# Optimization experiments

Hardware: AMD Instinct MI355X
Metric: run time of the kernel (lower is better)

Reference implementation:

```python
import jax, jax.numpy as jnp
import numpy as np

ALPHA_LINK = 2.0   # init arg alpha_link
TOP_K = 4096       # init arg top_k
BATCH = 65536
NUM_CLASSES = 4096


def setup_inputs() -> dict:
    key = jax.random.key(0)
    k1, k2, k3 = jax.random.split(key, 3)
    y_pred = jax.random.normal(k1, (BATCH, NUM_CLASSES), dtype=jnp.float32)
    y_true = jax.random.randint(k2, (BATCH,), 0, NUM_CLASSES, dtype=jnp.int32)
    # dense boolean link table: link_table[gt, pred] == True iff pred in link[gt]
    link_table = jax.random.randint(k3, (NUM_CLASSES, NUM_CLASSES), 0, 2, dtype=jnp.int32).astype(bool)
    return {"y_pred": y_pred, "y_true": y_true, "link_table": link_table}


def reference(y_pred, y_true, link_table):
    # vectorized replacement of the per-sample dict-lookup loop
    pred = jnp.argmax(y_pred, axis=1)                     # [B]
    linked = link_table[y_true, pred]                     # [B] bool
    # factor = alpha_link iff pred != gt and pred in link[gt]; else 1
    factor = jnp.where((pred != y_true) & linked, ALPHA_LINK, 1.0)
    # cross_entropy(reduction='none'), weight=None
    logp = jax.nn.log_softmax(y_pred, axis=1)             # [B, C]
    ce = -jnp.take_along_axis(logp, y_true[:, None], axis=1)[:, 0]  # [B]
    worst_k, _ = jax.lax.top_k(factor * ce, TOP_K)        # [TOP_K]
    return jnp.mean(worst_k)
```

## Files before the change

### kernel.cpp

```cpp
#include <hip/hip_runtime.h>

#define NCLS   4096
#define BATCHN 65536
#define TOPK   4096
#define ALPHA  2.0f

typedef float vfloat4 __attribute__((ext_vector_type(4)));

__global__ __launch_bounds__(256) void detect_and_zero_kernel(
    const unsigned int* __restrict__ lt, int* __restrict__ flag,
    unsigned int* __restrict__ ghist) {
    const int tid = threadIdx.x;
    #pragma unroll
    for (int i = 0; i < 16; ++i) ghist[i * 256 + tid] = 0u;
    if (tid < 64) {
        unsigned int bad = 0;
        for (int i = tid; i < 1024; i += 64) bad |= (lt[i] > 1u) ? 1u : 0u;
        unsigned long long mask = __ballot(bad != 0);
        if (tid == 0) flag[0] = (mask == 0ULL) ? 1 : 0;
    }
}

__device__ inline void amax_comb(float& m, int& mi, float om, int omi) {
    if (om > m || (om == m && omi < mi)) { m = om; mi = omi; }
}

__global__ __launch_bounds__(256) void row_loss_kernel(
    const float* __restrict__ yp, const int* __restrict__ yt,
    const unsigned char* __restrict__ lt, const int* __restrict__ flag,
    float* __restrict__ losses) {
    const int b   = blockIdx.x;
    const int tid = threadIdx.x;
    const vfloat4* row = reinterpret_cast<const vfloat4*>(yp + (size_t)b * NCLS);

    vfloat4 v0 = __builtin_nontemporal_load(&row[0 * 256 + tid]);
    vfloat4 v1 = __builtin_nontemporal_load(&row[1 * 256 + tid]);
    vfloat4 v2 = __builtin_nontemporal_load(&row[2 * 256 + tid]);
    vfloat4 v3 = __builtin_nontemporal_load(&row[3 * 256 + tid]);

    float m = -3.4e38f; int mi = 0;
    {
        const int c0 = tid * 4;
        if (v0.x > m) { m = v0.x; mi = c0 + 0; }
        if (v0.y > m) { m = v0.y; mi = c0 + 1; }
        if (v0.z > m) { m = v0.z; mi = c0 + 2; }
        if (v0.w > m) { m = v0.w; mi = c0 + 3; }
        const int c1 = 1024 + tid * 4;
        if (v1.x > m) { m = v1.x; mi = c1 + 0; }
        if (v1.y > m) { m = v1.y; mi = c1 + 1; }
        if (v1.z > m) { m = v1.z; mi = c1 + 2; }
        if (v1.w > m) { m = v1.w; mi = c1 + 3; }
        const int c2 = 2048 + tid * 4;
        if (v2.x > m) { m = v2.x; mi = c2 + 0; }
        if (v2.y > m) { m = v2.y; mi = c2 + 1; }
        if (v2.z > m) { m = v2.z; mi = c2 + 2; }
        if (v2.w > m) { m = v2.w; mi = c2 + 3; }
        const int c3 = 3072 + tid * 4;
        if (v3.x > m) { m = v3.x; mi = c3 + 0; }
        if (v3.y > m) { m = v3.y; mi = c3 + 1; }
        if (v3.z > m) { m = v3.z; mi = c3 + 2; }
        if (v3.w > m) { m = v3.w; mi = c3 + 3; }
    }

    #pragma unroll
    for (int off = 32; off > 0; off >>= 1) {
        float om  = __shfl_down(m, off, 64);
        int   omi = __shfl_down(mi, off, 64);
        amax_comb(m, mi, om, omi);
    }

    __shared__ float wmax[4];
    __shared__ int   wmi[4];
    __shared__ float wsum[4];
    __shared__ float s_M;
    __shared__ int   s_pred;
    __shared__ float s_true;

    const int wid = tid >> 6, lane = tid & 63;
    if (lane == 0) { wmax[wid] = m; wmi[wid] = mi; }
    __syncthreads();
    if (tid == 0) {
        float M = wmax[0]; int P = wmi[0];
        amax_comb(M, P, wmax[1], wmi[1]);
        amax_comb(M, P, wmax[2], wmi[2]);
        amax_comb(M, P, wmax[3], wmi[3]);
        s_M = M; s_pred = P;
    }
    __syncthreads();
    const float M = s_M;

    float sum = 0.f;
    sum += __expf(v0.x - M); sum += __expf(v0.y - M);
    sum += __expf(v0.z - M); sum += __expf(v0.w - M);
    sum += __expf(v1.x - M); sum += __expf(v1.y - M);
    sum += __expf(v1.z - M); sum += __expf(v1.w - M);
    sum += __expf(v2.x - M); sum += __expf(v2.y - M);
    sum += __expf(v2.z - M); sum += __expf(v2.w - M);
    sum += __expf(v3.x - M); sum += __expf(v3.y - M);
    sum += __expf(v3.z - M); sum += __expf(v3.w - M);

    #pragma unroll
    for (int off = 32; off > 0; off >>= 1) sum += __shfl_down(sum, off, 64);

    const int gt = yt[b];
    if (tid == ((gt >> 2) & 255)) {
        const int j = gt >> 10, k = gt & 3;
        vfloat4 vv = (j == 0) ? v0 : (j == 1) ? v1 : (j == 2) ? v2 : v3;
        float t = (k == 0) ? vv.x : (k == 1) ? vv.y : (k == 2) ? vv.z : vv.w;
        s_true = t;
    }
    if (lane == 0) wsum[wid] = sum;
    __syncthreads();

    if (tid == 0) {
        float tot = wsum[0] + wsum[1] + wsum[2] + wsum[3];
        float ce  = logf(tot) + s_M - s_true;
        int pred  = s_pred;
        float factor = 1.0f;
        if (pred != gt) {
            size_t idx = (size_t)gt * NCLS + (size_t)pred;
            int linked = flag[0] ? ((const int*)lt)[idx] : (int)lt[idx];
            if (linked) factor = ALPHA;
        }
        losses[b] = factor * ce;
    }
}

__global__ __launch_bounds__(1024) void hist_l1_kernel(
    const float* __restrict__ losses, unsigned int* __restrict__ ghist) {
    __shared__ unsigned int hist[4096];
    const int tid = threadIdx.x;
    for (int i = tid; i < 4096; i += 1024) hist[i] = 0;
    __syncthreads();
    const int base = blockIdx.x * 4096;
    #pragma unroll
    for (int k = 0; k < 4; ++k) {
        const unsigned int key = __float_as_uint(losses[base + k * 1024 + tid]);
        atomicAdd(&hist[key >> 20], 1u);
    }
    __syncthreads();
    for (int i = tid; i < 4096; i += 1024) {
        const unsigned int h = hist[i];
        if (h) atomicAdd(&ghist[i], h);
    }
}

__device__ inline void scan4096(const unsigned int* hist, unsigned int kneed,
                                int* s_bin, unsigned int* s_kneed, int tid) {
    if (tid < 64) {
        unsigned int sb = 0;
        #pragma unroll 8
        for (int i = 0; i < 64; ++i) sb += hist[tid * 64 + i];
        unsigned int GS = sb;
        #pragma unroll
        for (int off = 1; off < 64; off <<= 1) {
            unsigned int o = __shfl_down(GS, off, 64);
            GS += (tid + off < 64) ? o : 0u;
        }
        unsigned long long b1 = __ballot(GS >= kneed);
        const int sstar = 63 - __clzll(b1);
        const unsigned int A1 = (sstar < 63) ? __shfl(GS, sstar + 1, 64) : 0u;

        unsigned int W = hist[sstar * 64 + tid];
        #pragma unroll
        for (int off = 1; off < 64; off <<= 1) {
            unsigned int o = __shfl_down(W, off, 64);
            W += (tid + off < 64) ? o : 0u;
        }
        unsigned long long b2 = __ballot(A1 + W >= kneed);
        const int tstar = 63 - __clzll(b2);
        const unsigned int above = A1 + ((tstar < 63) ? __shfl(W, tstar + 1, 64) : 0u);
        if (tid == 0) { *s_bin = sstar * 64 + tstar; *s_kneed = kneed - above; }
    }
}

__global__ __launch_bounds__(1024) void topk_mean_kernel(
    const float* __restrict__ losses, const unsigned int* __restrict__ ghist,
    float* __restrict__ out) {
    __shared__ unsigned int hist[4096];
    __shared__ int          s_bin;
    __shared__ unsigned int s_kneed;
    __shared__ double       dsum[16];
    __shared__ unsigned int dcnt[16];

    const int tid = threadIdx.x;
    const int lane = tid & 63;
    const int N = BATCHN, K = TOPK;

    for (int i = tid; i < 4096; i += 1024) hist[i] = ghist[i];
    __syncthreads();
    scan4096(hist, (unsigned int)K, &s_bin, &s_kneed, tid);
    __syncthreads();
    const unsigned int t1 = (unsigned int)s_bin;
    const unsigned int k1 = s_kneed;
    __syncthreads();

    for (int i = tid; i < 4096; i += 1024) hist[i] = 0;
    __syncthreads();
    for (int i = tid; i < N; i += 1024) {
        const unsigned int key = __float_as_uint(losses[i]);
        if ((key >> 20) == t1) atomicAdd(&hist[(key >> 8) & 0xFFFu], 1u);
    }
    __syncthreads();
    scan4096(hist, k1, &s_bin, &s_kneed, tid);
    __syncthreads();
    const unsigned int t2 = (unsigned int)s_bin;
    const unsigned int k2 = s_kneed;
    const unsigned int pref = (t1 << 12) | t2;
    __syncthreads();

    for (int i = tid; i < 256; i += 1024) hist[i] = 0;
    __syncthreads();
    for (int i = tid; i < N; i += 1024) {
        const unsigned int key = __float_as_uint(losses[i]);
        if ((key >> 8) == pref) atomicAdd(&hist[key & 0xFFu], 1u);
    }
    __syncthreads();
    if (tid < 64) {
        unsigned int sb = hist[tid * 4] + hist[tid * 4 + 1] +
                          hist[tid * 4 + 2] + hist[tid * 4 + 3];
        unsigned int GS = sb;
        #pragma unroll
        for (int off = 1; off < 64; off <<= 1) {
            unsigned int o = __shfl_down(GS, off, 64);
            GS += (tid + off < 64) ? o : 0u;
        }
        unsigned long long b1 = __ballot(GS >= k2);
        const int sstar = 63 - __clzll(b1);
        const unsigned int A1 = (sstar < 63) ? __shfl(GS, sstar + 1, 64) : 0u;
        if (tid == 0) {
            unsigned int G = A1; int tstar = sstar * 4;
            for (int j = 3; j >= 0; --j) {
                const int bin = sstar * 4 + j;
                if (G + hist[bin] >= k2) { tstar = bin; break; }
                G += hist[bin];
            }
            s_bin = tstar;
        }
    }
    __syncthreads();
    const unsigned int T = (pref << 8) | (unsigned int)s_bin;

    double local = 0.0; unsigned int cgt = 0;
    for (int i = tid; i < N; i += 1024) {
        const unsigned int key = __float_as_uint(losses[i]);
        if (key > T) { local += (double)__uint_as_float(key); cgt++; }
    }
    const int wid = tid >> 6;
    #pragma unroll
    for (int off = 32; off > 0; off >>= 1) {
        local += __shfl_down(local, off, 64);
        cgt   += __shfl_down(cgt, off, 64);
    }
    if (lane == 0) { dsum[wid] = local; dcnt[wid] = cgt; }
    __syncthreads();
    if (tid == 0) {
        double tot = 0.0; unsigned int ngt = 0;
        for (int w = 0; w < 16; ++w) { tot += dsum[w]; ngt += dcnt[w]; }
        tot += (double)(K - ngt) * (double)__uint_as_float(T);
        out[0] = (float)(tot / (double)K);
    }
}

extern "C" void kernel_launch(void* const* d_in, const int* in_sizes, int n_in,
                              void* d_out, int out_size, void* d_ws, size_t ws_size,
                              hipStream_t stream) {
    const float* y_pred     = (const float*)d_in[0];
    const int* y_true       = (const int*)d_in[1];
    const unsigned char* lt = (const unsigned char*)d_in[2];
    float* out              = (float*)d_out;

    int*          flag   = (int*)d_ws;
    unsigned int* ghist  = (unsigned int*)((char*)d_ws + 1024);
    float*        losses = (float*)((char*)d_ws + 32768);

    detect_and_zero_kernel<<<1, 256, 0, stream>>>((const unsigned int*)lt, flag, ghist);
    row_loss_kernel<<<BATCHN, 256, 0, stream>>>(y_pred, y_true, lt, flag, losses);
    hist_l1_kernel<<<16, 1024, 0, stream>>>(losses, ghist);
    topk_mean_kernel<<<1, 1024, 0, stream>>>(losses, ghist, out);
}
```

Measured before the change: 206.0 us.

## Process two rows per block with online-softmax wave merge and one barrier

Each block now handles two batch rows, issuing all eight vector loads up front. Per-thread max and sum-of-exps are computed together, online-softmax style, and merged across the wave with xor shuffles. A single block barrier replaces the previous two-barrier max-then-sum sequence. This is meant to cut barrier latency and per-block overhead and to keep more loads in flight, at the cost of more registers per thread and half as many blocks.

Measured after the change: 211.4 us. 1.03x slower.

```diff
diff --git a/kernel.cpp b/kernel.cpp
--- a/kernel.cpp
+++ b/kernel.cpp
@@ -29,100 +29,150 @@
     const float* __restrict__ yp, const int* __restrict__ yt,
     const unsigned char* __restrict__ lt, const int* __restrict__ flag,
     float* __restrict__ losses) {
-    const int b   = blockIdx.x;
+    const int bA  = blockIdx.x * 2;
+    const int bB  = bA + 1;
     const int tid = threadIdx.x;
-    const vfloat4* row = reinterpret_cast<const vfloat4*>(yp + (size_t)b * NCLS);
-
-    vfloat4 v0 = __builtin_nontemporal_load(&row[0 * 256 + tid]);
-    vfloat4 v1 = __builtin_nontemporal_load(&row[1 * 256 + tid]);
-    vfloat4 v2 = __builtin_nontemporal_load(&row[2 * 256 + tid]);
-    vfloat4 v3 = __builtin_nontemporal_load(&row[3 * 256 + tid]);
-
-    float m = -3.4e38f; int mi = 0;
+    const int lane = tid & 63, wid = tid >> 6;
+
+    const vfloat4* rowA = reinterpret_cast<const vfloat4*>(yp + (size_t)bA * NCLS);
+    const vfloat4* rowB = reinterpret_cast<const vfloat4*>(yp + (size_t)bB * NCLS);
+
+    vfloat4 a0 = __builtin_nontemporal_load(&rowA[0 * 256 + tid]);
+    vfloat4 a1 = __builtin_nontemporal_load(&rowA[1 * 256 + tid]);
+    vfloat4 a2 = __builtin_nontemporal_load(&rowA[2 * 256 + tid]);
+    vfloat4 a3 = __builtin_nontemporal_load(&rowA[3 * 256 + tid]);
+    vfloat4 b0 = __builtin_nontemporal_load(&rowB[0 * 256 + tid]);
+    vfloat4 b1 = __builtin_nontemporal_load(&rowB[1 * 256 + tid]);
+    vfloat4 b2 = __builtin_nontemporal_load(&rowB[2 * 256 + tid]);
+    vfloat4 b3 = __builtin_nontemporal_load(&rowB[3 * 256 + tid]);
+
+    const int gtA = yt[bA];
+    const int gtB = yt[bB];
+
+    __shared__ float wmA[4], wsA[4]; __shared__ int wiA[4];
+    __shared__ float wmB[4], wsB[4]; __shared__ int wiB[4];
+    __shared__ float s_trueA, s_trueB;
+
+    const int base = tid * 4;
+
     {
-        const int c0 = tid * 4;
-        if (v0.x > m) { m = v0.x; mi = c0 + 0; }
-        if (v0.y > m) { m = v0.y; mi = c0 + 1; }
-        if (v0.z > m) { m = v0.z; mi = c0 + 2; }
-        if (v0.w > m) { m = v0.w; mi = c0 + 3; }
-        const int c1 = 1024 + tid * 4;
-        if (v1.x > m) { m = v1.x; mi = c1 + 0; }
-        if (v1.y > m) { m = v1.y; mi = c1 + 1; }
-        if (v1.z > m) { m = v1.z; mi = c1 + 2; }
-        if (v1.w > m) { m = v1.w; mi = c1 + 3; }
-        const int c2 = 2048 + tid * 4;
-        if (v2.x > m) { m = v2.x; mi = c2 + 0; }
-        if (v2.y > m) { m = v2.y; mi = c2 + 1; }
-        if (v2.z > m) { m = v2.z; mi = c2 + 2; }
-        if (v2.w > m) { m = v2.w; mi = c2 + 3; }
-        const int c3 = 3072 + tid * 4;
-        if (v3.x > m) { m = v3.x; mi = c3 + 0; }
-        if (v3.y > m) { m = v3.y; mi = c3 + 1; }
-        if (v3.z > m) { m = v3.z; mi = c3 + 2; }
-        if (v3.w > m) { m = v3.w; mi = c3 + 3; }
-    }
-
-    #pragma unroll
-    for (int off = 32; off > 0; off >>= 1) {
-        float om  = __shfl_down(m, off, 64);
-        int   omi = __shfl_down(mi, off, 64);
-        amax_comb(m, mi, om, omi);
-    }
-
-    __shared__ float wmax[4];
-    __shared__ int   wmi[4];
-    __shared__ float wsum[4];
-    __shared__ float s_M;
-    __shared__ int   s_pred;
-    __shared__ float s_true;
-
-    const int wid = tid >> 6, lane = tid & 63;
-    if (lane == 0) { wmax[wid] = m; wmi[wid] = mi; }
-    __syncthreads();
+        float m = a0.x; int mi = base;
+        if (a0.y > m) { m = a0.y; mi = base + 1; }
+        if (a0.z > m) { m = a0.z; mi = base + 2; }
+        if (a0.w > m) { m = a0.w; mi = base + 3; }
+        if (a1.x > m) { m = a1.x; mi = 1024 + base + 0; }
+        if (a1.y > m) { m = a1.y; mi = 1024 + base + 1; }
+        if (a1.z > m) { m = a1.z; mi = 1024 + base + 2; }
+        if (a1.w > m) { m = a1.w; mi = 1024 + base + 3; }
+        if (a2.x > m) { m = a2.x; mi = 2048 + base + 0; }
+        if (a2.y > m) { m = a2.y; mi = 2048 + base + 1; }
+        if (a2.z > m) { m = a2.z; mi = 2048 + base + 2; }
+        if (a2.w > m) { m = a2.w; mi = 2048 + base + 3; }
+        if (a3.x > m) { m = a3.x; mi = 3072 + base + 0; }
+        if (a3.y > m) { m = a3.y; mi = 3072 + base + 1; }
+        if (a3.z > m) { m = a3.z; mi = 3072 + base + 2; }
+        if (a3.w > m) { m = a3.w; mi = 3072 + base + 3; }
+
+        float sx = __expf(a0.x - m) + __expf(a1.x - m) + __expf(a2.x - m) + __expf(a3.x - m);
+        float sy = __expf(a0.y - m) + __expf(a1.y - m) + __expf(a2.y - m) + __expf(a3.y - m);
+        float sz = __expf(a0.z - m) + __expf(a1.z - m) + __expf(a2.z - m) + __expf(a3.z - m);
+        float sw = __expf(a0.w - m) + __expf(a1.w - m) + __expf(a2.w - m) + __expf(a3.w - m);
+        float s = (sx + sy) + (sz + sw);
+
+        if (tid == ((gtA >> 2) & 255)) {
+            const int j = gtA >> 10, k = gtA & 3;
+            vfloat4 vv = (j == 0) ? a0 : (j == 1) ? a1 : (j == 2) ? a2 : a3;
+            s_trueA = (k == 0) ? vv.x : (k == 1) ? vv.y : (k == 2) ? vv.z : vv.w;
+        }
+
+        float mw = m; int miw = mi;
+        #pragma unroll
+        for (int off = 32; off > 0; off >>= 1) {
+            float om  = __shfl_xor(mw, off, 64);
+            int   omi = __shfl_xor(miw, off, 64);
+            amax_comb(mw, miw, om, omi);
+        }
+        s *= __expf(m - mw);
+        #pragma unroll
+        for (int off = 32; off > 0; off >>= 1) s += __shfl_xor(s, off, 64);
+        if (lane == 0) { wmA[wid] = mw; wiA[wid] = miw; wsA[wid] = s; }
+    }
+
+    {
+        float m = b0.x; int mi = base;
+        if (b0.y > m) { m = b0.y; mi = base + 1; }
+        if (b0.z > m) { m = b0.z; mi = base + 2; }
+        if (b0.w > m) { m = b0.w; mi = base + 3; }
+        if (b1.x > m) { m = b1.x; mi = 1024 + base + 0; }
+        if (b1.y > m) { m = b1.y; mi = 1024 + base + 1; }
+        if (b1.z > m) { m = b1.z; mi = 1024 + base + 2; }
+        if (b1.w > m) { m = b1.w; mi = 1024 + base + 3; }
+        if (b2.x > m) { m = b2.x; mi = 2048 + base + 0; }
+        if (b2.y > m) { m = b2.y; mi = 2048 + base + 1; }
+        if (b2.z > m) { m = b2.z; mi = 2048 + base + 2; }
+        if (b2.w > m) { m = b2.w; mi = 2048 + base + 3; }
+        if (b3.x > m) { m = b3.x; mi = 3072 + base + 0; }
+        if (b3.y > m) { m = b3.y; mi = 3072 + base + 1; }
+        if (b3.z > m) { m = b3.z; mi = 3072 + base + 2; }
+        if (b3.w > m) { m = b3.w; mi = 3072 + base + 3; }
+
+        float sx = __expf(b0.x - m) + __expf(b1.x - m) + __expf(b2.x - m) + __expf(b3.x - m);
+        float sy = __expf(b0.y - m) + __expf(b1.y - m) + __expf(b2.y - m) + __expf(b3.y - m);
+        float sz = __expf(b0.z - m) + __expf(b1.z - m) + __expf(b2.z - m) + __expf(b3.z - m);
+        float sw = __expf(b0.w - m) + __expf(b1.w - m) + __expf(b2.w - m) + __expf(b3.w - m);
+        float s = (sx + sy) + (sz + sw);
+
+        if (tid == ((gtB >> 2) & 255)) {
+            const int j = gtB >> 10, k = gtB & 3;
+            vfloat4 vv = (j == 0) ? b0 : (j == 1) ? b1 : (j == 2) ? b2 : b3;
+            s_trueB = (k == 0) ? vv.x : (k == 1) ? vv.y : (k == 2) ? vv.z : vv.w;
+        }
+
+        float mw = m; int miw = mi;
+        #pragma unroll
+        for (int off = 32; off > 0; off >>= 1) {
+            float om  = __shfl_xor(mw, off, 64);
+            int   omi = __shfl_xor(miw, off, 64);
+            amax_comb(mw, miw, om, omi);
+        }
+        s *= __expf(m - mw);
+        #pragma unroll
+        for (int off = 32; off > 0; off >>= 1) s += __shfl_xor(s, off, 64);
+        if (lane == 0) { wmB[wid] = mw; wiB[wid] = miw; wsB[wid] = s; }
+    }
+
+    __syncthreads();
+
     if (tid == 0) {
-        float M = wmax[0]; int P = wmi[0];
-        amax_comb(M, P, wmax[1], wmi[1]);
-        amax_comb(M, P, wmax[2], wmi[2]);
-        amax_comb(M, P, wmax[3], wmi[3]);
-        s_M = M; s_pred = P;
-    }
-    __syncthreads();
-    const float M = s_M;
-
-    float sum = 0.f;
-    sum += __expf(v0.x - M); sum += __expf(v0.y - M);
-    sum += __expf(v0.z - M); sum += __expf(v0.w - M);
-    sum += __expf(v1.x - M); sum += __expf(v1.y - M);
-    sum += __expf(v1.z - M); sum += __expf(v1.w - M);
-    sum += __expf(v2.x - M); sum += __expf(v2.y - M);
-    sum += __expf(v2.z - M); sum += __expf(v2.w - M);
-    sum += __expf(v3.x - M); sum += __expf(v3.y - M);
-    sum += __expf(v3.z - M); sum += __expf(v3.w - M);
-
-    #pragma unroll
-    for (int off = 32; off > 0; off >>= 1) sum += __shfl_down(sum, off, 64);
-
-    const int gt = yt[b];
-    if (tid == ((gt >> 2) & 255)) {
-        const int j = gt >> 10, k = gt & 3;
-        vfloat4 vv = (j == 0) ? v0 : (j == 1) ? v1 : (j == 2) ? v2 : v3;
-        float t = (k == 0) ? vv.x : (k == 1) ? vv.y : (k == 2) ? vv.z : vv.w;
-        s_true = t;
-    }
-    if (lane == 0) wsum[wid] = sum;
-    __syncthreads();
-
-    if (tid == 0) {
-        float tot = wsum[0] + wsum[1] + wsum[2] + wsum[3];
-        float ce  = logf(tot) + s_M - s_true;
-        int pred  = s_pred;
+        float M = wmA[0]; int P = wiA[0];
+        amax_comb(M, P, wmA[1], wiA[1]);
+        amax_comb(M, P, wmA[2], wiA[2]);
+        amax_comb(M, P, wmA[3], wiA[3]);
+        const float tot = wsA[0] * __expf(wmA[0] - M) + wsA[1] * __expf(wmA[1] - M) +
+                          wsA[2] * __expf(wmA[2] - M) + wsA[3] * __expf(wmA[3] - M);
+        const float ce = logf(tot) + M - s_trueA;
         float factor = 1.0f;
-        if (pred != gt) {
-            size_t idx = (size_t)gt * NCLS + (size_t)pred;
-            int linked = flag[0] ? ((const int*)lt)[idx] : (int)lt[idx];
+        if (P != gtA) {
+            const size_t li = (size_t)gtA * NCLS + (size_t)P;
+            const int linked = flag[0] ? ((const int*)lt)[li] : (int)lt[li];
             if (linked) factor = ALPHA;
         }
-        losses[b] = factor * ce;
+        losses[bA] = factor * ce;
+    } else if (tid == 64) {
+        float M = wmB[0]; int P = wiB[0];
+        amax_comb(M, P, wmB[1], wiB[1]);
+        amax_comb(M, P, wmB[2], wiB[2]);
+        amax_comb(M, P, wmB[3], wiB[3]);
+        const float tot = wsB[0] * __expf(wmB[0] - M) + wsB[1] * __expf(wmB[1] - M) +
+                          wsB[2] * __expf(wmB[2] - M) + wsB[3] * __expf(wmB[3] - M);
+        const float ce = logf(tot) + M - s_trueB;
+        float factor = 1.0f;
+        if (P != gtB) {
+            const size_t li = (size_t)gtB * NCLS + (size_t)P;
+            const int linked = flag[0] ? ((const int*)lt)[li] : (int)lt[li];
+            if (linked) factor = ALPHA;
+        }
+        losses[bB] = factor * ce;
     }
 }
 
@@ -275,7 +325,7 @@
     float*        losses = (float*)((char*)d_ws + 32768);
 
     detect_and_zero_kernel<<<1, 256, 0, stream>>>((const unsigned int*)lt, flag, ghist);
-    row_loss_kernel<<<BATCHN, 256, 0, stream>>>(y_pred, y_true, lt, flag, losses);
+    row_loss_kernel<<<BATCHN / 2, 256, 0, stream>>>(y_pred, y_true, lt, flag, losses);
     hist_l1_kernel<<<16, 1024, 0, stream>>>(losses, ghist);
     topk_mean_kernel<<<1, 1024, 0, stream>>>(losses, ghist, out);
 }
```
